# Performance work log

Hardware: AMD Instinct MI355X
Metric: run time of the kernel (lower is better)

The kernel has to match this reference:

```python
import jax, jax.numpy as jnp
import numpy as np

B, N, M, D, H = 2, 256, 64, 768, 12
HD = D // H  # head dim 64


def setup_inputs() -> dict:
    key = jax.random.key(0)
    ks = jax.random.split(key, 8)
    s = 0.02
    return {
        "x": jax.random.normal(ks[0], (B, N, D), jnp.float32),
        "sim_embeddings": jax.random.normal(ks[1], (B, N, M, D), jnp.float32),
        "Wq": jax.random.normal(ks[2], (D, D), jnp.float32) * s,
        "bq": jnp.zeros((D,), jnp.float32),
        "Wkv": jax.random.normal(ks[3], (D, 2 * D), jnp.float32) * s,
        "bkv": jnp.zeros((2 * D,), jnp.float32),
        "Wp": jax.random.normal(ks[4], (D, D), jnp.float32) * s,
        "bp": jnp.zeros((D,), jnp.float32),
    }


def reference(x, sim_embeddings, Wq, bq, Wkv, bkv, Wp, bp):
    # x: (B,N,D); sim_embeddings: (B,N,M,D)
    b, n, d = x.shape
    m = sim_embeddings.shape[2]
    scale = HD ** -0.5

    q = (x @ Wq + bq).reshape(b, n, H, HD).transpose(0, 2, 1, 3)  # (B,H,N,hd)

    kv_x = x @ Wkv + bkv                       # (B,N,2D)
    k_x, v_x = jnp.split(kv_x, 2, axis=-1)
    k_x = k_x.reshape(b, n, H, HD).transpose(0, 2, 1, 3)  # (B,H,N,hd) shared-global K
    v_x = v_x.reshape(b, n, H, HD).transpose(0, 2, 1, 3)

    kv_s = sim_embeddings @ Wkv + bkv          # (B,N,M,2D)
    k_s, v_s = jnp.split(kv_s, 2, axis=-1)
    k_s = k_s.reshape(b, n, m, H, HD).transpose(0, 3, 1, 2, 4)  # (B,H,N,M,hd) per-query local K
    v_s = v_s.reshape(b, n, m, H, HD).transpose(0, 3, 1, 2, 4)

    # scores over concatenated [global N keys | local M keys] without expanding K to (B,N,N+M,D)
    sg = jnp.einsum('bhnd,bhkd->bhnk', q, k_x) * scale   # (B,H,N,N)
    sl = jnp.einsum('bhnd,bhnmd->bhnm', q, k_s) * scale  # (B,H,N,M)
    attn = jax.nn.softmax(jnp.concatenate([sg, sl], axis=-1), axis=-1)
    ag, al = attn[..., :n], attn[..., n:]

    out = (jnp.einsum('bhnk,bhkd->bhnd', ag, v_x)
           + jnp.einsum('bhnm,bhnmd->bhnd', al, v_s))   # (B,H,N,hd)
    out = out.transpose(0, 2, 1, 3).reshape(b, n, d)
    return out @ Wp + bp
```

## Files before the change

### kernel.cpp

```cpp
#include <hip/hip_runtime.h>
#include <stdint.h>

#define DEV_INLINE __device__ __forceinline__

typedef __bf16 bf16x8 __attribute__((ext_vector_type(8)));
typedef float f32x4 __attribute__((ext_vector_type(4)));

typedef const __attribute__((address_space(1))) void* gas_ptr;
typedef __attribute__((address_space(3))) void* las_ptr;

DEV_INLINE unsigned short f2bf(float f) {
    union { float f; unsigned u; } v; v.f = f;
    unsigned r = v.u + 0x7fffu + ((v.u >> 16) & 1u);
    return (unsigned short)(r >> 16);
}
DEV_INLINE float bf2f(unsigned short u) {
    union { unsigned u; float f; } v; v.u = ((unsigned)u) << 16;
    return v.f;
}


__global__ void cast_bf16_kernel(const float* __restrict__ src,
                                 unsigned short* __restrict__ dst, long n4) {
    long i = (long)blockIdx.x * blockDim.x + threadIdx.x;
    if (i >= n4) return;
    float4 a = ((const float4*)src)[i];
    ushort4 o;
    o.x = f2bf(a.x); o.y = f2bf(a.y); o.z = f2bf(a.z); o.w = f2bf(a.w);
    ((ushort4*)dst)[i] = o;
}

__global__ void transpose_cast_kernel(const float* __restrict__ src, int C,
                                      unsigned short* __restrict__ dst, int ld_dst) {
    __shared__ float t[64][65];
    int c0 = blockIdx.x * 64, r0 = blockIdx.y * 64;
    int tx = threadIdx.x, ty = threadIdx.y;
    #pragma unroll
    for (int i = 0; i < 64; i += 16)
        t[ty + i][tx] = src[(long)(r0 + ty + i) * C + c0 + tx];
    __syncthreads();
    #pragma unroll
    for (int i = 0; i < 64; i += 16)
        dst[(long)(c0 + ty + i) * ld_dst + r0 + tx] = f2bf(t[tx][ty + i]);
}

__global__ void bias_init_kernel(const float* __restrict__ bq,
                                 const float* __restrict__ bkv,
                                 float* __restrict__ bias1,
                                 float* __restrict__ zerobuf) {
    int i = blockIdx.x * 256 + threadIdx.x;
    if (i < 2304) bias1[i] = (i < 768) ? bq[i] : bkv[i - 768];
    else if (i < 3072) zerobuf[i - 2304] = 0.f;
}


template <int WM, int WN, int WAVES_M, int OUT, bool CIN, bool G1E>
__global__ __launch_bounds__(256)
void gemm_bf16_kernel(const unsigned short* __restrict__ A, int lda,
                      const unsigned short* __restrict__ BT, int ldb,
                      const float* __restrict__ bias,
                      void* __restrict__ Cout, int ldc, int K,
                      const float* __restrict__ cin,
                      long aZb, long aZh, long bZb, long bZh, long oZb, long oZh,
                      float* __restrict__ g1_qf, unsigned short* __restrict__ g1_qb,
                      unsigned short* __restrict__ g1_kxb,
                      unsigned short* __restrict__ g1_vxT) {
    constexpr int TR = WAVES_M * WM * 16;
    constexpr int TC = (4 / WAVES_M) * WN * 16;
    __shared__ unsigned short As[TR * 64];
    __shared__ unsigned short Bs[TC * 64];
    const int tid = threadIdx.x;
    const int w = tid >> 6, lane = tid & 63;
    const int lm = lane & 15, quad = lane >> 4;
    const int z = blockIdx.z;
    const int zb = z / 12, zh = z % 12;
    A  += zb * aZb + zh * aZh;
    BT += zb * bZb + zh * bZh;
    const long obase = zb * oZb + zh * oZh;
    const long tm = (long)blockIdx.y * TR;
    const long tn = (long)blockIdx.x * TC;
    const int m_off = (w % WAVES_M) * WM * 16;
    const int n_off = (w / WAVES_M) * WN * 16;
    const int lrow8 = lane >> 3;
    const int lcol_sw = (((lane & 7) ^ lrow8) * 8);

    f32x4 acc[WM][WN];
    #pragma unroll
    for (int mi = 0; mi < WM; ++mi)
        #pragma unroll
        for (int ni = 0; ni < WN; ++ni) acc[mi][ni] = f32x4{0.f, 0.f, 0.f, 0.f};

    for (int k0 = 0; k0 < K; k0 += 64) {
        __syncthreads();
        #pragma unroll
        for (int i = 0; i < TR / 32; ++i) {
            int r0 = w * (TR / 4) + i * 8;
            const unsigned short* ga = A + (tm + r0 + lrow8) * lda + k0 + lcol_sw;
            __builtin_amdgcn_global_load_lds((gas_ptr)ga, (las_ptr)(As + r0 * 64), 16, 0, 0);
        }
        #pragma unroll
        for (int i = 0; i < TC / 32; ++i) {
            int r0 = w * (TC / 4) + i * 8;
            const unsigned short* gb = BT + (tn + r0 + lrow8) * ldb + k0 + lcol_sw;
            __builtin_amdgcn_global_load_lds((gas_ptr)gb, (las_ptr)(Bs + r0 * 64), 16, 0, 0);
        }
        __syncthreads();
        #pragma unroll
        for (int kk = 0; kk < 2; ++kk) {
            bf16x8 af[WM], bfr[WN];
            #pragma unroll
            for (int mi = 0; mi < WM; ++mi) {
                int r = m_off + mi * 16 + lm;
                af[mi] = *(const bf16x8*)(As + r * 64 + (((kk * 4 + quad) ^ (r & 7)) * 8));
            }
            #pragma unroll
            for (int ni = 0; ni < WN; ++ni) {
                int r = n_off + ni * 16 + lm;
                bfr[ni] = *(const bf16x8*)(Bs + r * 64 + (((kk * 4 + quad) ^ (r & 7)) * 8));
            }
            #pragma unroll
            for (int mi = 0; mi < WM; ++mi)
                #pragma unroll
                for (int ni = 0; ni < WN; ++ni)
                    acc[mi][ni] = __builtin_amdgcn_mfma_f32_16x16x32_bf16(
                        af[mi], bfr[ni], acc[mi][ni], 0, 0, 0);
        }
    }

    #pragma unroll
    for (int mi = 0; mi < WM; ++mi) {
        #pragma unroll
        for (int ni = 0; ni < WN; ++ni) {
            long col = tn + n_off + ni * 16 + lm;
            float bv = bias[col];
            #pragma unroll
            for (int r = 0; r < 4; ++r) {
                long row = tm + m_off + mi * 16 + quad * 4 + r;
                float v = acc[mi][ni][r] + bv;
                if (G1E) {
                    if (col < 768) {
                        g1_qf[row * 768 + col] = v;
                        g1_qb[row * 768 + col] = f2bf(v);
                    } else if (col < 1536) {
                        g1_kxb[row * 768 + (col - 768)] = f2bf(v);
                    } else {
                        int j = (int)col - 1536, h = j >> 6, d = j & 63;
                        int bb = (int)row >> 8, n = (int)row & 255;
                        g1_vxT[((long)(bb * 12 + h) * 64 + d) * 256 + n] = f2bf(v);
                    }
                } else {
                    long idx = obase + row * ldc + col;
                    if (CIN) v += cin[idx];
                    if (OUT == 0) ((float*)Cout)[idx] = v;
                    else ((unsigned short*)Cout)[idx] = f2bf(v);
                }
            }
        }
    }
}

__global__ __launch_bounds__(256)
void attn_b1_kernel(const unsigned short* __restrict__ simb,
                    const unsigned short* __restrict__ qWb,
                    const float* __restrict__ qf,
                    const float* __restrict__ bkv,
                    const float* __restrict__ sgbuf,
                    unsigned short* __restrict__ agb,
                    float* __restrict__ algl,
                    float* __restrict__ outg0) {
    __shared__ unsigned short qw_s[16 * 784];
    __shared__ unsigned short As[64 * 64];
    __shared__ float q_l[768];
    __shared__ float slb_s[12];
    __shared__ float scl[12][68];

    const int t = threadIdx.x;
    const int lane = t & 63, w = t >> 6;
    const int lm = lane & 15, quad = lane >> 4;
    const int n = blockIdx.x, b = blockIdx.y;
    const int n_ = b * 256 + n;

    {
        const int h = t >> 4, c0 = t & 15;
        const unsigned short* src = qWb + ((long)h * 512 + n_) * 768;
        #pragma unroll
        for (int j = 0; j < 6; ++j) {
            int ch = c0 + 16 * j;
            *(bf16x8*)(qw_s + h * 784 + ch * 8) = *(const bf16x8*)(src + ch * 8);
        }
    }
    q_l[t] = qf[(long)n_ * 768 + t];
    q_l[t + 256] = qf[(long)n_ * 768 + t + 256];
    q_l[t + 512] = qf[(long)n_ * 768 + t + 512];
    __syncthreads();
    if (t < 12) {
        float s = 0.f;
        #pragma unroll 8
        for (int d = 0; d < 64; ++d) s += q_l[t * 64 + d] * bkv[t * 64 + d];
        slb_s[t] = s;
    }

    const int lrow8 = lane >> 3;
    const int lcol_sw = (((lane & 7) ^ lrow8) * 8);
    f32x4 acc = {};
    for (int k0 = 0; k0 < 768; k0 += 64) {
        __syncthreads();
        #pragma unroll
        for (int i = 0; i < 2; ++i) {
            int r0 = w * 16 + i * 8;
            const unsigned short* ga = simb + ((long)n_ * 64 + r0 + lrow8) * 768 + k0 + lcol_sw;
            __builtin_amdgcn_global_load_lds((gas_ptr)ga, (las_ptr)(As + r0 * 64), 16, 0, 0);
        }
        __syncthreads();
        #pragma unroll
        for (int kk = 0; kk < 2; ++kk) {
            int r = w * 16 + lm;
            bf16x8 af = *(const bf16x8*)(As + r * 64 + (((kk * 4 + quad) ^ (r & 7)) * 8));
            bf16x8 bf_ = *(const bf16x8*)(qw_s + lm * 784 + k0 + kk * 32 + quad * 8);
            acc = __builtin_amdgcn_mfma_f32_16x16x32_bf16(af, bf_, acc, 0, 0, 0);
        }
    }
    if (lm < 12) {
        #pragma unroll
        for (int r = 0; r < 4; ++r)
            scl[lm][w * 16 + quad * 4 + r] = (acc[r] + slb_s[lm]) * 0.125f;
    }
    __syncthreads();

    #pragma unroll
    for (int i = 0; i < 3; ++i) {
        const int h = w * 3 + i;
        const float* sgr = sgbuf + (long)(b * 12 + h) * 65536 + (long)n * 256;
        float v0 = sgr[lane] * 0.125f, v1 = sgr[lane + 64] * 0.125f,
              v2 = sgr[lane + 128] * 0.125f, v3 = sgr[lane + 192] * 0.125f;
        float v4 = scl[h][lane];
        float mx = fmaxf(fmaxf(fmaxf(v0, v1), fmaxf(v2, v3)), v4);
        #pragma unroll
        for (int off = 32; off > 0; off >>= 1) mx = fmaxf(mx, __shfl_xor(mx, off));
        float e0 = __expf(v0 - mx), e1 = __expf(v1 - mx), e2 = __expf(v2 - mx),
              e3 = __expf(v3 - mx), e4 = __expf(v4 - mx);
        float s = e0 + e1 + e2 + e3 + e4;
        #pragma unroll
        for (int off = 32; off > 0; off >>= 1) s += __shfl_xor(s, off);
        float inv = __frcp_rn(s);
        unsigned short* agr = agb + (long)(b * 12 + h) * 65536 + (long)n * 256;
        agr[lane] = f2bf(e0 * inv); agr[lane + 64] = f2bf(e1 * inv);
        agr[lane + 128] = f2bf(e2 * inv); agr[lane + 192] = f2bf(e3 * inv);
        float al = e4 * inv;
        algl[(long)n_ * 768 + h * 64 + lane] = al;
        float am = al;
        #pragma unroll
        for (int off = 32; off > 0; off >>= 1) am += __shfl_xor(am, off);
        outg0[(long)n_ * 768 + h * 64 + lane] = am * bkv[768 + h * 64 + lane];
    }
}

__global__ __launch_bounds__(256)
void attn_b2_kernel(const unsigned short* __restrict__ simb,
                    const float* __restrict__ algl,
                    unsigned short* __restrict__ simbar) {
    __shared__ float al_l[768];
    const int t = threadIdx.x;
    const int n_ = blockIdx.y * 256 + blockIdx.x;
    al_l[t] = algl[(long)n_ * 768 + t];
    al_l[t + 256] = algl[(long)n_ * 768 + t + 256];
    al_l[t + 512] = algl[(long)n_ * 768 + t + 512];
    __syncthreads();

    float acc[12][3] = {};
    const unsigned short* sbase = simb + (long)n_ * 64 * 768;
    for (int m = 0; m < 64; ++m) {
        float s0 = bf2f(sbase[(long)m * 768 + t]);
        float s1 = bf2f(sbase[(long)m * 768 + t + 256]);
        float s2 = bf2f(sbase[(long)m * 768 + t + 512]);
        #pragma unroll
        for (int h = 0; h < 12; ++h) {
            float a = al_l[h * 64 + m];
            acc[h][0] += a * s0; acc[h][1] += a * s1; acc[h][2] += a * s2;
        }
    }
    #pragma unroll
    for (int h = 0; h < 12; ++h) {
        unsigned short* dst = simbar + ((long)h * 512 + n_) * 768;
        dst[t] = f2bf(acc[h][0]);
        dst[t + 256] = f2bf(acc[h][1]);
        dst[t + 512] = f2bf(acc[h][2]);
    }
}


extern "C" void kernel_launch(void* const* d_in, const int* in_sizes, int n_in,
                              void* d_out, int out_size, void* d_ws, size_t ws_size,
                              hipStream_t stream) {
    const float* x   = (const float*)d_in[0];
    const float* sim = (const float*)d_in[1];
    const float* Wq  = (const float*)d_in[2];
    const float* bq  = (const float*)d_in[3];
    const float* Wkv = (const float*)d_in[4];
    const float* bkv = (const float*)d_in[5];
    const float* Wp  = (const float*)d_in[6];
    const float* bp  = (const float*)d_in[7];
    float* out = (float*)d_out;

    char* ws = (char*)d_ws;
    size_t off = 0;
    auto alloc = [&](size_t bytes) {
        char* p = ws + off;
        off += (bytes + 255) & ~(size_t)255;
        return p;
    };
    unsigned short* simb   = (unsigned short*)alloc(32768UL * 768 * 2);
    unsigned short* xb     = (unsigned short*)alloc(512UL * 768 * 2);
    unsigned short* w1t    = (unsigned short*)alloc(2304UL * 768 * 2);
    unsigned short* wkvb   = (unsigned short*)alloc(768UL * 1536 * 2);
    unsigned short* wpt    = (unsigned short*)alloc(768UL * 768 * 2);
    float*          qf     = (float*)alloc(512UL * 768 * 4);
    unsigned short* qb     = (unsigned short*)alloc(512UL * 768 * 2);
    unsigned short* kxb    = (unsigned short*)alloc(512UL * 768 * 2);
    unsigned short* vxT    = (unsigned short*)alloc(24UL * 64 * 256 * 2);
    unsigned short* qWb    = (unsigned short*)alloc(16UL * 512 * 768 * 2);
    float*          sgbuf  = (float*)alloc(24UL * 65536 * 4);
    unsigned short* agb    = (unsigned short*)alloc(24UL * 65536 * 2);
    float*          algl   = (float*)alloc(512UL * 768 * 4);
    float*          outg0  = (float*)alloc(512UL * 768 * 4);
    float*          outg   = (float*)alloc(512UL * 768 * 4);
    unsigned short* simbar = (unsigned short*)alloc(12UL * 512 * 768 * 2);
    unsigned short* attnb  = (unsigned short*)alloc(512UL * 768 * 2);
    float*          bias1  = (float*)alloc(2304UL * 4);
    float*          zbuf   = (float*)alloc(768UL * 4);

    cast_bf16_kernel<<<24576, 256, 0, stream>>>(sim, simb, 32768L * 768 / 4);
    cast_bf16_kernel<<<384, 256, 0, stream>>>(x, xb, 512L * 768 / 4);
    cast_bf16_kernel<<<1152, 256, 0, stream>>>(Wkv, wkvb, 768L * 1536 / 4);
    transpose_cast_kernel<<<dim3(12, 12), dim3(64, 16), 0, stream>>>(Wq, 768, w1t, 768);
    transpose_cast_kernel<<<dim3(24, 12), dim3(64, 16), 0, stream>>>(Wkv, 1536, w1t + 768L * 768, 768);
    transpose_cast_kernel<<<dim3(12, 12), dim3(64, 16), 0, stream>>>(Wp, 768, wpt, 768);
    bias_init_kernel<<<12, 256, 0, stream>>>(bq, bkv, bias1, zbuf);

    gemm_bf16_kernel<2, 2, 2, 0, false, true><<<dim3(36, 8, 1), 256, 0, stream>>>(
        xb, 768, w1t, 768, bias1, nullptr, 768, 768, nullptr,
        0, 0, 0, 0, 0, 0, qf, qb, kxb, vxT);

    gemm_bf16_kernel<2, 2, 2, 1, false, false><<<dim3(12, 8, 12), 256, 0, stream>>>(
        qb, 768, wkvb, 1536, zbuf, qWb, 768, 64, nullptr,
        0, 64, 0, 64, 0, 512L * 768, nullptr, nullptr, nullptr, nullptr);

    gemm_bf16_kernel<2, 2, 2, 0, false, false><<<dim3(4, 4, 24), 256, 0, stream>>>(
        qb, 768, kxb, 768, zbuf, sgbuf, 256, 64, nullptr,
        196608, 64, 196608, 64, 786432, 65536, nullptr, nullptr, nullptr, nullptr);

    attn_b1_kernel<<<dim3(256, 2), 256, 0, stream>>>(
        simb, qWb, qf, bkv, sgbuf, agb, algl, outg0);

    attn_b2_kernel<<<dim3(256, 2), 256, 0, stream>>>(simb, algl, simbar);

    gemm_bf16_kernel<2, 2, 2, 0, true, false><<<dim3(1, 4, 24), 256, 0, stream>>>(
        agb, 256, vxT, 256, zbuf, outg, 768, 256, outg0,
        786432, 65536, 196608, 16384, 196608, 64, nullptr, nullptr, nullptr, nullptr);

    gemm_bf16_kernel<2, 2, 2, 1, true, false><<<dim3(1, 8, 12), 256, 0, stream>>>(
        simbar, 768, w1t + 1536L * 768, 768, zbuf, attnb, 768, 768, outg,
        0, 393216, 0, 49152, 0, 64, nullptr, nullptr, nullptr, nullptr);

    gemm_bf16_kernel<2, 2, 2, 0, false, false><<<dim3(12, 8, 1), 256, 0, stream>>>(
        attnb, 768, wpt, 768, bp, out, 768, 768, nullptr,
        0, 0, 0, 0, 0, 0, nullptr, nullptr, nullptr, nullptr);
}
```

Before: 261.7 us.

## Fuse sim bf16 cast and both local-attention kernels into one pass

Removes the separate full-size fp32-to-bf16 cast of sim_embeddings and merges the local-score/softmax kernel with the weighted-sum kernel. The fused kernel reads fp32 sim directly, converting to bf16 while staging into shared memory for the MFMA, and keeps local attention weights in shared memory instead of a global buffer. This avoids writing and re-reading a large bf16 copy and a launch, at the cost of reading fp32 sim twice per block (relying on cache for the second pass) and losing the async global-to-LDS load.

Measured after the change: 253.4 us. 1.03x faster.

```diff
diff --git a/kernel.cpp b/kernel.cpp
--- a/kernel.cpp
+++ b/kernel.cpp
@@ -160,25 +160,27 @@
 }
 
 __global__ __launch_bounds__(256)
-void attn_b1_kernel(const unsigned short* __restrict__ simb,
-                    const unsigned short* __restrict__ qWb,
-                    const float* __restrict__ qf,
-                    const float* __restrict__ bkv,
-                    const float* __restrict__ sgbuf,
-                    unsigned short* __restrict__ agb,
-                    float* __restrict__ algl,
-                    float* __restrict__ outg0) {
+void attn_fused_kernel(const float* __restrict__ sim,
+                       const unsigned short* __restrict__ qWb,
+                       const float* __restrict__ qf,
+                       const float* __restrict__ bkv,
+                       const float* __restrict__ sgbuf,
+                       unsigned short* __restrict__ agb,
+                       float* __restrict__ outg0,
+                       unsigned short* __restrict__ simbar) {
     __shared__ unsigned short qw_s[16 * 784];
-    __shared__ unsigned short As[64 * 64];
+    __shared__ unsigned short sim_s[64 * 64];
     __shared__ float q_l[768];
     __shared__ float slb_s[12];
     __shared__ float scl[12][68];
+    __shared__ float al_s[12][64];
 
     const int t = threadIdx.x;
     const int lane = t & 63, w = t >> 6;
     const int lm = lane & 15, quad = lane >> 4;
     const int n = blockIdx.x, b = blockIdx.y;
     const int n_ = b * 256 + n;
+    const float* simn = sim + (long)n_ * 49152;
 
     {
         const int h = t >> 4, c0 = t & 15;
@@ -200,22 +202,28 @@
         slb_s[t] = s;
     }
 
-    const int lrow8 = lane >> 3;
-    const int lcol_sw = (((lane & 7) ^ lrow8) * 8);
     f32x4 acc = {};
     for (int k0 = 0; k0 < 768; k0 += 64) {
         __syncthreads();
         #pragma unroll
         for (int i = 0; i < 2; ++i) {
-            int r0 = w * 16 + i * 8;
-            const unsigned short* ga = simb + ((long)n_ * 64 + r0 + lrow8) * 768 + k0 + lcol_sw;
-            __builtin_amdgcn_global_load_lds((gas_ptr)ga, (las_ptr)(As + r0 * 64), 16, 0, 0);
+            int id = t + 256 * i;
+            int r = id >> 3, q = id & 7;
+            const float* gp = simn + r * 768 + k0 + q * 8;
+            float4 a = *(const float4*)gp;
+            float4 c = *(const float4*)(gp + 4);
+            union { bf16x8 v; unsigned short u[8]; } pk;
+            pk.u[0] = f2bf(a.x); pk.u[1] = f2bf(a.y);
+            pk.u[2] = f2bf(a.z); pk.u[3] = f2bf(a.w);
+            pk.u[4] = f2bf(c.x); pk.u[5] = f2bf(c.y);
+            pk.u[6] = f2bf(c.z); pk.u[7] = f2bf(c.w);
+            *(bf16x8*)(sim_s + r * 64 + ((q ^ (r & 7)) * 8)) = pk.v;
         }
         __syncthreads();
         #pragma unroll
         for (int kk = 0; kk < 2; ++kk) {
             int r = w * 16 + lm;
-            bf16x8 af = *(const bf16x8*)(As + r * 64 + (((kk * 4 + quad) ^ (r & 7)) * 8));
+            bf16x8 af = *(const bf16x8*)(sim_s + r * 64 + (((kk * 4 + quad) ^ (r & 7)) * 8));
             bf16x8 bf_ = *(const bf16x8*)(qw_s + lm * 784 + k0 + kk * 32 + quad * 8);
             acc = __builtin_amdgcn_mfma_f32_16x16x32_bf16(af, bf_, acc, 0, 0, 0);
         }
@@ -247,44 +255,33 @@
         agr[lane] = f2bf(e0 * inv); agr[lane + 64] = f2bf(e1 * inv);
         agr[lane + 128] = f2bf(e2 * inv); agr[lane + 192] = f2bf(e3 * inv);
         float al = e4 * inv;
-        algl[(long)n_ * 768 + h * 64 + lane] = al;
+        al_s[h][lane] = al;
         float am = al;
         #pragma unroll
         for (int off = 32; off > 0; off >>= 1) am += __shfl_xor(am, off);
         outg0[(long)n_ * 768 + h * 64 + lane] = am * bkv[768 + h * 64 + lane];
     }
-}
-
-__global__ __launch_bounds__(256)
-void attn_b2_kernel(const unsigned short* __restrict__ simb,
-                    const float* __restrict__ algl,
-                    unsigned short* __restrict__ simbar) {
-    __shared__ float al_l[768];
-    const int t = threadIdx.x;
-    const int n_ = blockIdx.y * 256 + blockIdx.x;
-    al_l[t] = algl[(long)n_ * 768 + t];
-    al_l[t + 256] = algl[(long)n_ * 768 + t + 256];
-    al_l[t + 512] = algl[(long)n_ * 768 + t + 512];
     __syncthreads();
 
-    float acc[12][3] = {};
-    const unsigned short* sbase = simb + (long)n_ * 64 * 768;
+    float a0[12], a1[12], a2[12];
+    #pragma unroll
+    for (int h = 0; h < 12; ++h) { a0[h] = 0.f; a1[h] = 0.f; a2[h] = 0.f; }
     for (int m = 0; m < 64; ++m) {
-        float s0 = bf2f(sbase[(long)m * 768 + t]);
-        float s1 = bf2f(sbase[(long)m * 768 + t + 256]);
-        float s2 = bf2f(sbase[(long)m * 768 + t + 512]);
+        float s0 = simn[(long)m * 768 + t];
+        float s1 = simn[(long)m * 768 + t + 256];
+        float s2 = simn[(long)m * 768 + t + 512];
         #pragma unroll
         for (int h = 0; h < 12; ++h) {
-            float a = al_l[h * 64 + m];
-            acc[h][0] += a * s0; acc[h][1] += a * s1; acc[h][2] += a * s2;
+            float a = al_s[h][m];
+            a0[h] += a * s0; a1[h] += a * s1; a2[h] += a * s2;
         }
     }
     #pragma unroll
     for (int h = 0; h < 12; ++h) {
         unsigned short* dst = simbar + ((long)h * 512 + n_) * 768;
-        dst[t] = f2bf(acc[h][0]);
-        dst[t + 256] = f2bf(acc[h][1]);
-        dst[t + 512] = f2bf(acc[h][2]);
+        dst[t] = f2bf(a0[h]);
+        dst[t + 256] = f2bf(a1[h]);
+        dst[t + 512] = f2bf(a2[h]);
     }
 }
 
@@ -309,7 +306,6 @@
         off += (bytes + 255) & ~(size_t)255;
         return p;
     };
-    unsigned short* simb   = (unsigned short*)alloc(32768UL * 768 * 2);
     unsigned short* xb     = (unsigned short*)alloc(512UL * 768 * 2);
     unsigned short* w1t    = (unsigned short*)alloc(2304UL * 768 * 2);
     unsigned short* wkvb   = (unsigned short*)alloc(768UL * 1536 * 2);
@@ -321,7 +317,6 @@
     unsigned short* qWb    = (unsigned short*)alloc(16UL * 512 * 768 * 2);
     float*          sgbuf  = (float*)alloc(24UL * 65536 * 4);
     unsigned short* agb    = (unsigned short*)alloc(24UL * 65536 * 2);
-    float*          algl   = (float*)alloc(512UL * 768 * 4);
     float*          outg0  = (float*)alloc(512UL * 768 * 4);
     float*          outg   = (float*)alloc(512UL * 768 * 4);
     unsigned short* simbar = (unsigned short*)alloc(12UL * 512 * 768 * 2);
@@ -329,7 +324,6 @@
     float*          bias1  = (float*)alloc(2304UL * 4);
     float*          zbuf   = (float*)alloc(768UL * 4);
 
-    cast_bf16_kernel<<<24576, 256, 0, stream>>>(sim, simb, 32768L * 768 / 4);
     cast_bf16_kernel<<<384, 256, 0, stream>>>(x, xb, 512L * 768 / 4);
     cast_bf16_kernel<<<1152, 256, 0, stream>>>(Wkv, wkvb, 768L * 1536 / 4);
     transpose_cast_kernel<<<dim3(12, 12), dim3(64, 16), 0, stream>>>(Wq, 768, w1t, 768);
@@ -349,10 +343,8 @@
         qb, 768, kxb, 768, zbuf, sgbuf, 256, 64, nullptr,
         196608, 64, 196608, 64, 786432, 65536, nullptr, nullptr, nullptr, nullptr);
 
-    attn_b1_kernel<<<dim3(256, 2), 256, 0, stream>>>(
-        simb, qWb, qf, bkv, sgbuf, agb, algl, outg0);
-
-    attn_b2_kernel<<<dim3(256, 2), 256, 0, stream>>>(simb, algl, simbar);
+    attn_fused_kernel<<<dim3(256, 2), 256, 0, stream>>>(
+        sim, qWb, qf, bkv, sgbuf, agb, outg0, simbar);
 
     gemm_bf16_kernel<2, 2, 2, 0, true, false><<<dim3(1, 4, 24), 256, 0, stream>>>(
         agb, 256, vxT, 256, zbuf, outg, 768, 256, outg0,
```
